# Performance work log

Measured on AMD Instinct MI355X. Metric: run time of the kernel, lower is better.

Reference implementation:

```python
import jax, jax.numpy as jnp
import numpy as np

D_MODEL = 1024
NUM_HEADS = 16
D_K = D_MODEL // NUM_HEADS
NEG = jnp.float32(-1e9)  # finite stand-in for -inf to keep softmax NaN-free on fully masked rows


def setup_inputs() -> dict:
    key = jax.random.key(0)
    ks = jax.random.split(key, 7)
    B, N_q, N_kv = 2, 2048, 2048
    x = jax.random.normal(ks[0], (B, N_q, D_MODEL), dtype=jnp.float32)
    K = jax.random.normal(ks[1], (B, NUM_HEADS, N_kv, D_K), dtype=jnp.float32)
    V = jax.random.normal(ks[2], (B, NUM_HEADS, N_kv, D_K), dtype=jnp.float32)
    # pad masks: True = keep. Ensure first kv position is always valid.
    kv_pad_mask = jax.random.uniform(ks[3], (B, 1, 1, N_kv)) > 0.1
    kv_pad_mask = kv_pad_mask.at[..., 0].set(True)
    q_pad_mask = jax.random.uniform(ks[4], (B, 1, N_q, 1)) > 0.1
    # params (torch Linear, bias=False); stored as [in, out] so y = x @ W
    Wq = jax.random.normal(ks[5], (D_MODEL, D_MODEL), dtype=jnp.float32) / np.sqrt(D_MODEL)
    Wo = jax.random.normal(ks[6], (D_MODEL, D_MODEL), dtype=jnp.float32) / np.sqrt(D_MODEL)
    return {"x": x, "K": K, "V": V, "Wq": Wq, "Wo": Wo,
            "kv_pad_mask": kv_pad_mask, "q_pad_mask": q_pad_mask}


def reference(x, K, V, Wq, Wo, kv_pad_mask, q_pad_mask):
    B, N_q, D = x.shape
    H, d_k = NUM_HEADS, D_K
    # Q projection and split into heads: [B, H, N_q, d_k]
    Q = (x @ Wq).reshape(B, N_q, H, d_k).transpose(0, 2, 1, 3)
    scores = jnp.einsum('bhqd,bhkd->bhqk', Q, K) / np.sqrt(d_k).astype(np.float32)
    keep = q_pad_mask & kv_pad_mask  # broadcast to [B,1,N_q,N_kv]
    scores = jnp.where(keep, scores, NEG)
    probs = jax.nn.softmax(scores, axis=-1)
    attn = jnp.einsum('bhqk,bhkd->bhqd', probs, V)  # [B,H,N_q,d_k]
    attn = attn.transpose(0, 2, 1, 3).reshape(B, N_q, H * d_k)
    return attn @ Wo
```

## Files before the change

### kernel.cpp

```cpp
#include <hip/hip_runtime.h>
#include <hip/hip_bf16.h>
#include <stdint.h>

typedef __hip_bfloat16 bf16;
typedef __attribute__((ext_vector_type(8))) short short8;
typedef __attribute__((ext_vector_type(4))) short s16x4;
typedef __attribute__((ext_vector_type(4))) float floatx4;

#define MFMA16(a, b, c) __builtin_amdgcn_mfma_f32_16x16x32_bf16(a, b, c, 0, 0, 0)
#define WAIT_VM4 3956
#define WAIT_VM0 3952

__device__ __forceinline__ void async_lds16(const void* g, void* l) {
  __builtin_amdgcn_global_load_lds((__attribute__((address_space(1))) const void*)g,
                                   (__attribute__((address_space(3))) void*)l, 16, 0, 0);
}

__device__ __forceinline__ unsigned rne2(float a, float b) {
  unsigned ua = __float_as_uint(a), ub = __float_as_uint(b);
  ua = ua + 0x7FFFu + ((ua >> 16) & 1u);
  ub = ub + 0x7FFFu + ((ub >> 16) & 1u);
  return (ua >> 16) | (ub & 0xFFFF0000u);
}

__global__ __launch_bounds__(256) void prep_k(const float* __restrict__ x, bf16* __restrict__ xb,
                                              const float* __restrict__ Kf, bf16* __restrict__ Kb,
                                              const float* __restrict__ Wq, bf16* __restrict__ WqT,
                                              const float* __restrict__ Wo, bf16* __restrict__ WoT,
                                              const float* __restrict__ V, bf16* __restrict__ VTb,
                                              const int* __restrict__ kvm, const int* __restrict__ qm,
                                              float* __restrict__ kvB, float* __restrict__ qB) {
  __shared__ float tile[64][65];
  int bid = blockIdx.x, tid = threadIdx.x;
  if (bid < 8192) {
    const float* s; bf16* d; int g = bid;
    if (g < 4096) { s = x; d = xb; } else { s = Kf; d = Kb; g -= 4096; }
    int i = (g * 256 + tid) * 4;
    float4 v = *(const float4*)(s + i);
    uint2 o = {rne2(v.x, v.y), rne2(v.z, v.w)};
    *(uint2*)(d + i) = o;
    return;
  }
  if (bid < 9744 - 16) {
    const float* s; bf16* d; int r0, c0, R, C;
    if (bid < 8704) {
      int idx = bid - 8192;
      s = (idx >> 8) ? Wo : Wq; d = (idx >> 8) ? WoT : WqT;
      int rem = idx & 255;
      r0 = (rem & 15) * 64; c0 = (rem >> 4) * 64; R = 1024; C = 1024;
    } else {
      int idx = bid - 8704;
      int m = idx >> 5;
      s = V + (size_t)m * 2048 * 64; d = VTb + (size_t)m * 2048 * 64;
      r0 = (idx & 31) * 64; c0 = 0; R = 2048; C = 64;
    }
    int tr = tid >> 2, tg = tid & 3;
#pragma unroll
    for (int k = 0; k < 4; ++k) {
      int col = tg * 16 + k * 4;
      float4 v = *(const float4*)(s + (size_t)(r0 + tr) * C + c0 + col);
      tile[tr][col] = v.x; tile[tr][col + 1] = v.y;
      tile[tr][col + 2] = v.z; tile[tr][col + 3] = v.w;
    }
    __syncthreads();
    int orow = tid >> 2, ch = tid & 3;
    bf16* drow = d + (size_t)(c0 + orow) * R + r0;
    uint4 w0, w1;
    w0.x = rne2(tile[ch * 8 + 0][orow], tile[ch * 8 + 1][orow]);
    w0.y = rne2(tile[ch * 8 + 2][orow], tile[ch * 8 + 3][orow]);
    w0.z = rne2(tile[ch * 8 + 4][orow], tile[ch * 8 + 5][orow]);
    w0.w = rne2(tile[ch * 8 + 6][orow], tile[ch * 8 + 7][orow]);
    w1.x = rne2(tile[32 + ch * 8 + 0][orow], tile[32 + ch * 8 + 1][orow]);
    w1.y = rne2(tile[32 + ch * 8 + 2][orow], tile[32 + ch * 8 + 3][orow]);
    w1.z = rne2(tile[32 + ch * 8 + 4][orow], tile[32 + ch * 8 + 5][orow]);
    w1.w = rne2(tile[32 + ch * 8 + 6][orow], tile[32 + ch * 8 + 7][orow]);
    *(uint4*)(drow + ch * 8) = w0;
    *(uint4*)(drow + 32 + ch * 8) = w1;
    return;
  }
  int i = (bid - (9744 - 16)) * 256 + tid;
  kvB[i] = kvm[i] ? 0.0f : -3000.0f;
  qB[i]  = qm[i]  ? 0.0f : -3000.0f;
}

__device__ __forceinline__ void storeC(bf16* C, size_t i, float v) { C[i] = __float2bfloat16(v); }
__device__ __forceinline__ void storeC(float* C, size_t i, float v) { C[i] = v; }

template <typename OT>
__global__ __launch_bounds__(256) void gemm_bt_k(const bf16* __restrict__ A,
                                                 const bf16* __restrict__ BT,
                                                 OT* __restrict__ C,
                                                 int M, int N, int K, float scale) {
  __shared__ __align__(16) bf16 As[2][64 * 64];
  __shared__ __align__(16) bf16 Bs[2][64 * 64];
  int tid = threadIdx.x;
  int wave = tid >> 6, lane = tid & 63;
  int quad = lane >> 4, lm = lane & 15;
  int wm = wave >> 1, wn = wave & 1;
  int row0 = blockIdx.y * 64, col0 = blockIdx.x * 64;

  floatx4 acc[2][2];
#pragma unroll
  for (int mt = 0; mt < 2; ++mt)
#pragma unroll
    for (int nt = 0; nt < 2; ++nt) acc[mt][nt] = (floatx4){0.f, 0.f, 0.f, 0.f};

  auto stageAB = [&](int buf, int k0) {
#pragma unroll
    for (int ch = 0; ch < 2; ++ch) {
      int e = (wave * 2 + ch) * 512 + lane * 8;
      int r = e >> 6, c16 = (e & 63) >> 3;
      int sc = (c16 ^ (r & 7)) * 8;
      async_lds16(A + (size_t)(row0 + r) * K + k0 + sc, &As[buf][(wave * 2 + ch) * 512]);
      async_lds16(BT + (size_t)(col0 + r) * K + k0 + sc, &Bs[buf][(wave * 2 + ch) * 512]);
    }
  };

  int niter = K >> 6;
  stageAB(0, 0);
  for (int i = 0; i < niter; ++i) {
    __builtin_amdgcn_s_barrier();
    if (i + 1 < niter) {
      stageAB((i + 1) & 1, (i + 1) << 6);
      __builtin_amdgcn_s_waitcnt(WAIT_VM4);
    } else {
      __builtin_amdgcn_s_waitcnt(WAIT_VM0);
    }
    __builtin_amdgcn_s_barrier();
    const bf16* Ac = As[i & 1];
    const bf16* Bc = Bs[i & 1];
    int sw = lm & 7;
#pragma unroll
    for (int ks = 0; ks < 64; ks += 32) {
      short8 af[2], bfr[2];
#pragma unroll
      for (int mt = 0; mt < 2; ++mt) {
        int R = wm * 32 + mt * 16 + lm;
        af[mt] = *(const short8*)&Ac[R * 64 + ((((ks >> 3) + quad) ^ sw) * 8)];
      }
#pragma unroll
      for (int nt = 0; nt < 2; ++nt) {
        int R = wn * 32 + nt * 16 + lm;
        bfr[nt] = *(const short8*)&Bc[R * 64 + ((((ks >> 3) + quad) ^ sw) * 8)];
      }
#pragma unroll
      for (int mt = 0; mt < 2; ++mt)
#pragma unroll
        for (int nt = 0; nt < 2; ++nt)
          acc[mt][nt] = MFMA16(af[mt], bfr[nt], acc[mt][nt]);
    }
  }
#pragma unroll
  for (int mt = 0; mt < 2; ++mt)
#pragma unroll
    for (int nt = 0; nt < 2; ++nt)
#pragma unroll
      for (int j = 0; j < 4; ++j) {
        int rr = row0 + wm * 32 + mt * 16 + quad * 4 + j;
        int cc = col0 + wn * 32 + nt * 16 + lm;
        storeC(C, (size_t)rr * N + cc, acc[mt][nt][j] * scale);
      }
}

__global__ __launch_bounds__(256, 4) void attn_k(const bf16* __restrict__ Q,
                                                 const bf16* __restrict__ Km,
                                                 const bf16* __restrict__ VT,
                                                 const float* __restrict__ qB,
                                                 const float* __restrict__ kvB,
                                                 bf16* __restrict__ O) {
  const float TINY = 9.313225746154785e-10f;
  __shared__ __align__(16) bf16 Ks[2][64 * 64];
  __shared__ __align__(16) bf16 Vs[2][64 * 64];
  __shared__ __align__(16) float kvBs[2048];

  int tid = threadIdx.x;
  int wave = tid >> 6, lane = tid & 63;
  int quad = lane >> 4, lm = lane & 15;
  int qb = blockIdx.x, h = blockIdx.y, b = blockIdx.z;
  int q0 = qb * 64 + wave * 16;

  const bf16* kbase = Km + (size_t)(b * 16 + h) * 2048 * 64;
  const bf16* vbase = VT + (size_t)(b * 16 + h) * 64 * 2048;
  const float* kvBb = kvB + b * 2048;

  {
    float4 v0 = *(const float4*)(kvBb + tid * 8);
    float4 v1 = *(const float4*)(kvBb + tid * 8 + 4);
    *(float4*)&kvBs[tid * 8] = v0;
    *(float4*)&kvBs[tid * 8 + 4] = v1;
  }

  short8 aq0, aq1;
  float qbias;
  {
    const bf16* qp = Q + (size_t)(b * 2048 + q0 + lm) * 1024 + h * 64 + quad * 8;
    aq0 = *(const short8*)qp;
    aq1 = *(const short8*)(qp + 32);
    qbias = qB[b * 2048 + q0 + lm];
  }

  short8 ones;
#pragma unroll
  for (int i = 0; i < 8; ++i) ones[i] = (short)0x3F80;

  floatx4 o_acc[4];
  floatx4 l_acc = (floatx4){0.f, 0.f, 0.f, 0.f};
#pragma unroll
  for (int t = 0; t < 4; ++t) o_acc[t] = (floatx4){0.f, 0.f, 0.f, 0.f};

  union S8U { short8 s8; s16x4 h[2]; unsigned u[4]; };

  auto stageKV = [&](int buf, int kv0) {
#pragma unroll
    for (int c = 0; c < 2; ++c) {
      int o = (wave * 2 + c) * 1024 + lane * 16;
      int r = o >> 7;
      int g16 = (o >> 4) & 7;
      int sc = ((g16 ^ (r & 7)) * 8);
      async_lds16(kbase + (size_t)(kv0 + r) * 64 + sc, &Ks[buf][(wave * 2 + c) * 512]);
      async_lds16(vbase + (size_t)r * 2048 + kv0 + sc, &Vs[buf][(wave * 2 + c) * 512]);
    }
  };

  __syncthreads();
  stageKV(0, 0);
  for (int i = 0; i < 32; ++i) {
    int kv0 = i * 64;
    __builtin_amdgcn_s_barrier();
    if (i + 1 < 32) {
      stageKV((i + 1) & 1, kv0 + 64);
      __builtin_amdgcn_s_waitcnt(WAIT_VM4);
    } else {
      __builtin_amdgcn_s_waitcnt(WAIT_VM0);
    }
    __builtin_amdgcn_s_barrier();
    const bf16* Kc = Ks[i & 1];
    const bf16* Vc = Vs[i & 1];

    S8U pf[2];
#pragma unroll
    for (int t = 0; t < 4; ++t) {
      int R = t * 16 + lm, sw = lm & 7;
      short8 kf0 = *(const short8*)&Kc[R * 64 + ((quad ^ sw) * 8)];
      short8 kf1 = *(const short8*)&Kc[R * 64 + (((quad + 4) ^ sw) * 8)];
      floatx4 z = *(const floatx4*)&kvBs[kv0 + t * 16 + quad * 4];
#pragma unroll
      for (int j = 0; j < 4; ++j) z[j] += qbias;
      z = MFMA16(kf0, aq0, z);
      z = MFMA16(kf1, aq1, z);
      float p0 = __builtin_amdgcn_exp2f(z[0]) + TINY;
      float p1 = __builtin_amdgcn_exp2f(z[1]) + TINY;
      float p2 = __builtin_amdgcn_exp2f(z[2]) + TINY;
      float p3 = __builtin_amdgcn_exp2f(z[3]) + TINY;
      pf[t >> 1].u[(t & 1) * 2 + 0] = rne2(p0, p1);
      pf[t >> 1].u[(t & 1) * 2 + 1] = rne2(p2, p3);
    }
#pragma unroll
    for (int t = 0; t < 4; ++t) {
      int D = t * 16 + lm, sw = lm & 7;
      int hoff = (quad & 1) * 4, qh = quad >> 1;
      S8U vf0, vf1;
      vf0.h[0] = *(const s16x4*)&Vc[D * 64 + (((0 + qh) ^ sw) * 8) + hoff];
      vf0.h[1] = *(const s16x4*)&Vc[D * 64 + (((2 + qh) ^ sw) * 8) + hoff];
      vf1.h[0] = *(const s16x4*)&Vc[D * 64 + (((4 + qh) ^ sw) * 8) + hoff];
      vf1.h[1] = *(const s16x4*)&Vc[D * 64 + (((6 + qh) ^ sw) * 8) + hoff];
      o_acc[t] = MFMA16(vf0.s8, pf[0].s8, o_acc[t]);
      o_acc[t] = MFMA16(vf1.s8, pf[1].s8, o_acc[t]);
    }
    l_acc = MFMA16(ones, pf[0].s8, l_acc);
    l_acc = MFMA16(ones, pf[1].s8, l_acc);
  }
  float rl = 1.0f / l_acc[0];
  bf16* orow = O + (size_t)(b * 2048 + q0 + lm) * 1024 + h * 64;
#pragma unroll
  for (int t = 0; t < 4; ++t) {
    uint2 ov = {rne2(o_acc[t][0] * rl, o_acc[t][1] * rl),
                rne2(o_acc[t][2] * rl, o_acc[t][3] * rl)};
    *(uint2*)(orow + t * 16 + quad * 4) = ov;
  }
}

extern "C" void kernel_launch(void* const* d_in, const int* in_sizes, int n_in,
                              void* d_out, int out_size, void* d_ws, size_t ws_size,
                              hipStream_t stream) {
  const float* x  = (const float*)d_in[0];
  const float* K  = (const float*)d_in[1];
  const float* V  = (const float*)d_in[2];
  const float* Wq = (const float*)d_in[3];
  const float* Wo = (const float*)d_in[4];
  const int* kvm  = (const int*)d_in[5];
  const int* qm   = (const int*)d_in[6];

  char* w = (char*)d_ws;
  bf16* xb    = (bf16*)(w);
  bf16* attnb = xb;
  bf16* Qb    = (bf16*)(w + (8u << 20));
  bf16* Kb    = (bf16*)(w + (16u << 20));
  bf16* VTb   = (bf16*)(w + (24u << 20));
  bf16* WqT   = (bf16*)(w + (32u << 20));
  bf16* WoT   = (bf16*)(w + (34u << 20));
  float* qB   = (float*)(w + (36u << 20));
  float* kvB  = (float*)(w + (36u << 20) + 16384);

  const float SCL2 = 0.18033688011112042f;

  prep_k<<<9744, 256, 0, stream>>>(x, xb, K, Kb, Wq, WqT, Wo, WoT, V, VTb, kvm, qm, kvB, qB);
  gemm_bt_k<bf16><<<dim3(16, 64), 256, 0, stream>>>(xb, WqT, Qb, 4096, 1024, 1024, SCL2);
  attn_k<<<dim3(32, 16, 2), 256, 0, stream>>>(Qb, Kb, VTb, qB, kvB, attnb);
  gemm_bt_k<float><<<dim3(16, 64), 256, 0, stream>>>(attnb, WoT, (float*)d_out, 4096, 1024, 1024, 1.0f);
}
```

Measured before the change: 200.8 us.

## Split attention over KV halves with 32-row waves and enlarge GEMM M tile

The attention kernel now gives each wave 32 query rows, so every K/V tile loaded into LDS feeds two query groups. The KV range is split into two 1024-wide slices that write unnormalised partial outputs and row sums, and a new combine kernel sums and normalises them. The GEMMs move to 128x64 tiles to get more MFMA work per staged B tile. In exchange there is an extra kernel launch, extra global traffic for the bf16 partials, higher register pressure, and half as many GEMM blocks.

```diff
diff --git a/kernel.cpp b/kernel.cpp
--- a/kernel.cpp
+++ b/kernel.cpp
@@ -8,6 +8,7 @@
 typedef __attribute__((ext_vector_type(4))) float floatx4;
 
 #define MFMA16(a, b, c) __builtin_amdgcn_mfma_f32_16x16x32_bf16(a, b, c, 0, 0, 0)
+#define WAIT_VM6 3958
 #define WAIT_VM4 3956
 #define WAIT_VM0 3952
 
@@ -91,38 +92,44 @@
                                                  const bf16* __restrict__ BT,
                                                  OT* __restrict__ C,
                                                  int M, int N, int K, float scale) {
-  __shared__ __align__(16) bf16 As[2][64 * 64];
+  __shared__ __align__(16) bf16 As[2][128 * 64];
   __shared__ __align__(16) bf16 Bs[2][64 * 64];
   int tid = threadIdx.x;
   int wave = tid >> 6, lane = tid & 63;
   int quad = lane >> 4, lm = lane & 15;
   int wm = wave >> 1, wn = wave & 1;
-  int row0 = blockIdx.y * 64, col0 = blockIdx.x * 64;
-
-  floatx4 acc[2][2];
-#pragma unroll
-  for (int mt = 0; mt < 2; ++mt)
+  int row0 = blockIdx.y * 128, col0 = blockIdx.x * 64;
+
+  floatx4 acc[4][2];
+#pragma unroll
+  for (int mt = 0; mt < 4; ++mt)
 #pragma unroll
     for (int nt = 0; nt < 2; ++nt) acc[mt][nt] = (floatx4){0.f, 0.f, 0.f, 0.f};
 
-  auto stageAB = [&](int buf, int k0) {
+  auto stage = [&](int buf, int k0) {
+#pragma unroll
+    for (int ch = 0; ch < 4; ++ch) {
+      int e = (wave * 4 + ch) * 512 + lane * 8;
+      int r = e >> 6, c16 = (e & 63) >> 3;
+      int sc = (c16 ^ (r & 7)) * 8;
+      async_lds16(A + (size_t)(row0 + r) * K + k0 + sc, &As[buf][(wave * 4 + ch) * 512]);
+    }
 #pragma unroll
     for (int ch = 0; ch < 2; ++ch) {
       int e = (wave * 2 + ch) * 512 + lane * 8;
       int r = e >> 6, c16 = (e & 63) >> 3;
       int sc = (c16 ^ (r & 7)) * 8;
-      async_lds16(A + (size_t)(row0 + r) * K + k0 + sc, &As[buf][(wave * 2 + ch) * 512]);
       async_lds16(BT + (size_t)(col0 + r) * K + k0 + sc, &Bs[buf][(wave * 2 + ch) * 512]);
     }
   };
 
   int niter = K >> 6;
-  stageAB(0, 0);
+  stage(0, 0);
   for (int i = 0; i < niter; ++i) {
     __builtin_amdgcn_s_barrier();
     if (i + 1 < niter) {
-      stageAB((i + 1) & 1, (i + 1) << 6);
-      __builtin_amdgcn_s_waitcnt(WAIT_VM4);
+      stage((i + 1) & 1, (i + 1) << 6);
+      __builtin_amdgcn_s_waitcnt(WAIT_VM6);
     } else {
       __builtin_amdgcn_s_waitcnt(WAIT_VM0);
     }
@@ -132,10 +139,10 @@
     int sw = lm & 7;
 #pragma unroll
     for (int ks = 0; ks < 64; ks += 32) {
-      short8 af[2], bfr[2];
-#pragma unroll
-      for (int mt = 0; mt < 2; ++mt) {
-        int R = wm * 32 + mt * 16 + lm;
+      short8 af[4], bfr[2];
+#pragma unroll
+      for (int mt = 0; mt < 4; ++mt) {
+        int R = wm * 64 + mt * 16 + lm;
         af[mt] = *(const short8*)&Ac[R * 64 + ((((ks >> 3) + quad) ^ sw) * 8)];
       }
 #pragma unroll
@@ -144,19 +151,19 @@
         bfr[nt] = *(const short8*)&Bc[R * 64 + ((((ks >> 3) + quad) ^ sw) * 8)];
       }
 #pragma unroll
-      for (int mt = 0; mt < 2; ++mt)
+      for (int mt = 0; mt < 4; ++mt)
 #pragma unroll
         for (int nt = 0; nt < 2; ++nt)
           acc[mt][nt] = MFMA16(af[mt], bfr[nt], acc[mt][nt]);
     }
   }
 #pragma unroll
-  for (int mt = 0; mt < 2; ++mt)
+  for (int mt = 0; mt < 4; ++mt)
 #pragma unroll
     for (int nt = 0; nt < 2; ++nt)
 #pragma unroll
       for (int j = 0; j < 4; ++j) {
-        int rr = row0 + wm * 32 + mt * 16 + quad * 4 + j;
+        int rr = row0 + wm * 64 + mt * 16 + quad * 4 + j;
         int cc = col0 + wn * 32 + nt * 16 + lm;
         storeC(C, (size_t)rr * N + cc, acc[mt][nt][j] * scale);
       }
@@ -167,46 +174,52 @@
                                                  const bf16* __restrict__ VT,
                                                  const float* __restrict__ qB,
                                                  const float* __restrict__ kvB,
-                                                 bf16* __restrict__ O) {
+                                                 bf16* __restrict__ Opart,
+                                                 float* __restrict__ lpart) {
   const float TINY = 9.313225746154785e-10f;
   __shared__ __align__(16) bf16 Ks[2][64 * 64];
   __shared__ __align__(16) bf16 Vs[2][64 * 64];
-  __shared__ __align__(16) float kvBs[2048];
+  __shared__ __align__(16) float kvBs[1024];
 
   int tid = threadIdx.x;
   int wave = tid >> 6, lane = tid & 63;
   int quad = lane >> 4, lm = lane & 15;
-  int qb = blockIdx.x, h = blockIdx.y, b = blockIdx.z;
-  int q0 = qb * 64 + wave * 16;
+  int qb = blockIdx.x & 15, slice = blockIdx.x >> 4;
+  int h = blockIdx.y, b = blockIdx.z;
+  int q0 = qb * 128 + wave * 32;
+  int kvbeg = slice * 1024;
 
   const bf16* kbase = Km + (size_t)(b * 16 + h) * 2048 * 64;
   const bf16* vbase = VT + (size_t)(b * 16 + h) * 64 * 2048;
   const float* kvBb = kvB + b * 2048;
 
   {
-    float4 v0 = *(const float4*)(kvBb + tid * 8);
-    float4 v1 = *(const float4*)(kvBb + tid * 8 + 4);
-    *(float4*)&kvBs[tid * 8] = v0;
-    *(float4*)&kvBs[tid * 8 + 4] = v1;
-  }
-
-  short8 aq0, aq1;
-  float qbias;
-  {
-    const bf16* qp = Q + (size_t)(b * 2048 + q0 + lm) * 1024 + h * 64 + quad * 8;
-    aq0 = *(const short8*)qp;
-    aq1 = *(const short8*)(qp + 32);
-    qbias = qB[b * 2048 + q0 + lm];
+    float4 v0 = *(const float4*)(kvBb + kvbeg + tid * 4);
+    *(float4*)&kvBs[tid * 4] = v0;
+  }
+
+  short8 aq[2][2];
+  float qbias[2];
+#pragma unroll
+  for (int g = 0; g < 2; ++g) {
+    const bf16* qp = Q + (size_t)(b * 2048 + q0 + g * 16 + lm) * 1024 + h * 64 + quad * 8;
+    aq[g][0] = *(const short8*)qp;
+    aq[g][1] = *(const short8*)(qp + 32);
+    qbias[g] = qB[b * 2048 + q0 + g * 16 + lm];
   }
 
   short8 ones;
 #pragma unroll
   for (int i = 0; i < 8; ++i) ones[i] = (short)0x3F80;
 
-  floatx4 o_acc[4];
-  floatx4 l_acc = (floatx4){0.f, 0.f, 0.f, 0.f};
-#pragma unroll
-  for (int t = 0; t < 4; ++t) o_acc[t] = (floatx4){0.f, 0.f, 0.f, 0.f};
+  floatx4 o_acc[2][4];
+  floatx4 l_acc[2];
+#pragma unroll
+  for (int g = 0; g < 2; ++g) {
+    l_acc[g] = (floatx4){0.f, 0.f, 0.f, 0.f};
+#pragma unroll
+    for (int t = 0; t < 4; ++t) o_acc[g][t] = (floatx4){0.f, 0.f, 0.f, 0.f};
+  }
 
   union S8U { short8 s8; s16x4 h[2]; unsigned u[4]; };
 
@@ -222,38 +235,30 @@
     }
   };
 
-  __syncthreads();
-  stageKV(0, 0);
-  for (int i = 0; i < 32; ++i) {
-    int kv0 = i * 64;
-    __builtin_amdgcn_s_barrier();
-    if (i + 1 < 32) {
-      stageKV((i + 1) & 1, kv0 + 64);
-      __builtin_amdgcn_s_waitcnt(WAIT_VM4);
-    } else {
-      __builtin_amdgcn_s_waitcnt(WAIT_VM0);
-    }
-    __builtin_amdgcn_s_barrier();
-    const bf16* Kc = Ks[i & 1];
-    const bf16* Vc = Vs[i & 1];
-
-    S8U pf[2];
+  auto compute = [&](int buf, int rel) {
+    const bf16* Kc = Ks[buf];
+    const bf16* Vc = Vs[buf];
+    S8U pf[2][2];
 #pragma unroll
     for (int t = 0; t < 4; ++t) {
       int R = t * 16 + lm, sw = lm & 7;
       short8 kf0 = *(const short8*)&Kc[R * 64 + ((quad ^ sw) * 8)];
       short8 kf1 = *(const short8*)&Kc[R * 64 + (((quad + 4) ^ sw) * 8)];
-      floatx4 z = *(const floatx4*)&kvBs[kv0 + t * 16 + quad * 4];
-#pragma unroll
-      for (int j = 0; j < 4; ++j) z[j] += qbias;
-      z = MFMA16(kf0, aq0, z);
-      z = MFMA16(kf1, aq1, z);
-      float p0 = __builtin_amdgcn_exp2f(z[0]) + TINY;
-      float p1 = __builtin_amdgcn_exp2f(z[1]) + TINY;
-      float p2 = __builtin_amdgcn_exp2f(z[2]) + TINY;
-      float p3 = __builtin_amdgcn_exp2f(z[3]) + TINY;
-      pf[t >> 1].u[(t & 1) * 2 + 0] = rne2(p0, p1);
-      pf[t >> 1].u[(t & 1) * 2 + 1] = rne2(p2, p3);
+      floatx4 zb = *(const floatx4*)&kvBs[rel + t * 16 + quad * 4];
+#pragma unroll
+      for (int g = 0; g < 2; ++g) {
+        floatx4 z;
+#pragma unroll
+        for (int j = 0; j < 4; ++j) z[j] = zb[j] + qbias[g];
+        z = MFMA16(kf0, aq[g][0], z);
+        z = MFMA16(kf1, aq[g][1], z);
+        float p0 = __builtin_amdgcn_exp2f(z[0]) + TINY;
+        float p1 = __builtin_amdgcn_exp2f(z[1]) + TINY;
+        float p2 = __builtin_amdgcn_exp2f(z[2]) + TINY;
+        float p3 = __builtin_amdgcn_exp2f(z[3]) + TINY;
+        pf[g][t >> 1].u[(t & 1) * 2 + 0] = rne2(p0, p1);
+        pf[g][t >> 1].u[(t & 1) * 2 + 1] = rne2(p2, p3);
+      }
     }
 #pragma unroll
     for (int t = 0; t < 4; ++t) {
@@ -264,20 +269,74 @@
       vf0.h[1] = *(const s16x4*)&Vc[D * 64 + (((2 + qh) ^ sw) * 8) + hoff];
       vf1.h[0] = *(const s16x4*)&Vc[D * 64 + (((4 + qh) ^ sw) * 8) + hoff];
       vf1.h[1] = *(const s16x4*)&Vc[D * 64 + (((6 + qh) ^ sw) * 8) + hoff];
-      o_acc[t] = MFMA16(vf0.s8, pf[0].s8, o_acc[t]);
-      o_acc[t] = MFMA16(vf1.s8, pf[1].s8, o_acc[t]);
-    }
-    l_acc = MFMA16(ones, pf[0].s8, l_acc);
-    l_acc = MFMA16(ones, pf[1].s8, l_acc);
-  }
-  float rl = 1.0f / l_acc[0];
-  bf16* orow = O + (size_t)(b * 2048 + q0 + lm) * 1024 + h * 64;
-#pragma unroll
-  for (int t = 0; t < 4; ++t) {
-    uint2 ov = {rne2(o_acc[t][0] * rl, o_acc[t][1] * rl),
-                rne2(o_acc[t][2] * rl, o_acc[t][3] * rl)};
-    *(uint2*)(orow + t * 16 + quad * 4) = ov;
-  }
+#pragma unroll
+      for (int g = 0; g < 2; ++g) {
+        o_acc[g][t] = MFMA16(vf0.s8, pf[g][0].s8, o_acc[g][t]);
+        o_acc[g][t] = MFMA16(vf1.s8, pf[g][1].s8, o_acc[g][t]);
+      }
+    }
+#pragma unroll
+    for (int g = 0; g < 2; ++g) {
+      l_acc[g] = MFMA16(ones, pf[g][0].s8, l_acc[g]);
+      l_acc[g] = MFMA16(ones, pf[g][1].s8, l_acc[g]);
+    }
+  };
+
+  __syncthreads();
+  stageKV(0, kvbeg);
+  for (int i = 0; i < 16; i += 2) {
+    __builtin_amdgcn_s_barrier();
+    stageKV(1, kvbeg + (i + 1) * 64);
+    __builtin_amdgcn_s_waitcnt(WAIT_VM4);
+    __builtin_amdgcn_s_barrier();
+    compute(0, i * 64);
+
+    __builtin_amdgcn_s_barrier();
+    if (i + 2 < 16) {
+      stageKV(0, kvbeg + (i + 2) * 64);
+      __builtin_amdgcn_s_waitcnt(WAIT_VM4);
+    } else {
+      __builtin_amdgcn_s_waitcnt(WAIT_VM0);
+    }
+    __builtin_amdgcn_s_barrier();
+    compute(1, (i + 1) * 64);
+  }
+  bf16* Op = Opart + (size_t)slice * 4194304u;
+#pragma unroll
+  for (int g = 0; g < 2; ++g) {
+    int q = b * 2048 + q0 + g * 16 + lm;
+    bf16* orow = Op + (size_t)q * 1024 + h * 64;
+#pragma unroll
+    for (int t = 0; t < 4; ++t) {
+      uint2 ov = {rne2(o_acc[g][t][0], o_acc[g][t][1]),
+                  rne2(o_acc[g][t][2], o_acc[g][t][3])};
+      *(uint2*)(orow + t * 16 + quad * 4) = ov;
+    }
+    if (quad == 0)
+      lpart[((size_t)slice * 4096 + (size_t)q) * 16 + h] = l_acc[g][0];
+  }
+}
+
+__global__ void combine_k(const bf16* __restrict__ Opart, const float* __restrict__ lpart,
+                          bf16* __restrict__ out) {
+  int i = (blockIdx.x * 256 + threadIdx.x) * 8;
+  int bq = i >> 10, h = (i >> 6) & 15;
+  float l = lpart[bq * 16 + h] + lpart[65536 + bq * 16 + h];
+  float rl = 1.0f / l;
+  float acc[8];
+#pragma unroll
+  for (int e = 0; e < 8; ++e) acc[e] = 0.f;
+#pragma unroll
+  for (int s = 0; s < 2; ++s) {
+    uint4 u = *(const uint4*)(Opart + s * 4194304 + i);
+    acc[0] += __uint_as_float(u.x << 16); acc[1] += __uint_as_float(u.x & 0xFFFF0000u);
+    acc[2] += __uint_as_float(u.y << 16); acc[3] += __uint_as_float(u.y & 0xFFFF0000u);
+    acc[4] += __uint_as_float(u.z << 16); acc[5] += __uint_as_float(u.z & 0xFFFF0000u);
+    acc[6] += __uint_as_float(u.w << 16); acc[7] += __uint_as_float(u.w & 0xFFFF0000u);
+  }
+  uint4 o = {rne2(acc[0] * rl, acc[1] * rl), rne2(acc[2] * rl, acc[3] * rl),
+             rne2(acc[4] * rl, acc[5] * rl), rne2(acc[6] * rl, acc[7] * rl)};
+  *(uint4*)(out + i) = o;
 }
 
 extern "C" void kernel_launch(void* const* d_in, const int* in_sizes, int n_in,
@@ -301,11 +360,14 @@
   bf16* WoT   = (bf16*)(w + (34u << 20));
   float* qB   = (float*)(w + (36u << 20));
   float* kvB  = (float*)(w + (36u << 20) + 16384);
+  bf16* Opart = (bf16*)(w + (40u << 20));
+  float* lpart = (float*)(w + (72u << 20));
 
   const float SCL2 = 0.18033688011112042f;
 
   prep_k<<<9744, 256, 0, stream>>>(x, xb, K, Kb, Wq, WqT, Wo, WoT, V, VTb, kvm, qm, kvB, qB);
-  gemm_bt_k<bf16><<<dim3(16, 64), 256, 0, stream>>>(xb, WqT, Qb, 4096, 1024, 1024, SCL2);
-  attn_k<<<dim3(32, 16, 2), 256, 0, stream>>>(Qb, Kb, VTb, qB, kvB, attnb);
-  gemm_bt_k<float><<<dim3(16, 64), 256, 0, stream>>>(attnb, WoT, (float*)d_out, 4096, 1024, 1024, 1.0f);
-}
+  gemm_bt_k<bf16><<<dim3(16, 32), 256, 0, stream>>>(xb, WqT, Qb, 4096, 1024, 1024, SCL2);
+  attn_k<<<dim3(32, 16, 2), 256, 0, stream>>>(Qb, Kb, VTb, qB, kvB, Opart, lpart);
+  combine_k<<<2048, 256, 0, stream>>>(Opart, lpart, attnb);
+  gemm_bt_k<float><<<dim3(16, 32), 256, 0, stream>>>(attnb, WoT, (float*)d_out, 4096, 1024, 1024, 1.0f);
+}
```

Result: slower. 206.8 us (+3.0%).
